# Optimization experiments

Measured on AMD Instinct MI355X. Metric: run time of the kernel, lower is better.

The kernel has to match this reference:

```python
import jax, jax.numpy as jnp
import numpy as np

NEG_INF = -1e30  # stands in for float('-inf'); avoids nan in masked softmax edge cases


def setup_inputs() -> dict:
    key = jax.random.key(0)
    ks = jax.random.split(key, 6)
    B, N, MD, QD, AD = 64, 512, 1024, 1024, 1024
    stdv_m = 1.0 / np.sqrt(MD)
    stdv_q = 1.0 / np.sqrt(QD)
    stdv_a = 1.0 / np.sqrt(AD)
    return {
        "memory_values": jax.random.normal(ks[0], (B, N, MD), dtype=jnp.float32),
        "mask": jax.random.randint(ks[1], (B, N), 0, 2, dtype=jnp.int32),
        "query": jax.random.normal(ks[2], (B, QD), dtype=jnp.float32),
        "Wh": jax.random.uniform(ks[3], (MD, AD), jnp.float32, -stdv_m, stdv_m),
        "Ws": jax.random.uniform(ks[4], (QD, AD), jnp.float32, -stdv_q, stdv_q),
        "v": jax.random.uniform(ks[5], (AD, 1), jnp.float32, -stdv_a, stdv_a),
    }


def reference(memory_values, mask, query, Wh, Ws, v):
    # Et(i) = tanh(Hi*Wh + St*Ws) @ v ; At = softmax(Et) with masking
    tq = query @ Ws                                   # (B, AD)
    h = jnp.tanh(memory_values @ Wh + tq[:, None, :])  # (B, N, AD)
    logits = jnp.squeeze(h @ v, axis=-1)              # (B, N)

    maskf = mask.astype(logits.dtype)
    # no_cells[b] == 1 iff every cell in row b is masked out
    no_cells = jnp.prod(1.0 - maskf, axis=1, keepdims=True)  # (B, 1)
    suppress = jnp.where(maskf == 0, NEG_INF, 0.0)
    suppress = jnp.where(no_cells == 1.0, 0.0, suppress)
    weights = jax.nn.softmax(logits + suppress, axis=-1)
    weights = jnp.where(no_cells == 1.0, 0.0, weights)

    context = jnp.einsum("bn,bnd->bd", weights, memory_values)
    return context
```

## Files before the change

### kernel.cpp

```cpp
#include <hip/hip_runtime.h>
#include <cstdint>
#include <cstddef>

typedef float floatx4 __attribute__((ext_vector_type(4)));
typedef _Float16 half8_t __attribute__((ext_vector_type(8)));
typedef _Float16 half2_t __attribute__((ext_vector_type(2)));

#define AS1 __attribute__((address_space(1)))
#define AS3 __attribute__((address_space(3)))

__device__ __forceinline__ void glds16(const void* g, void* l) {
  __builtin_amdgcn_global_load_lds((const AS1 void*)g, (AS3 void*)l, 16, 0, 0);
}

__device__ __forceinline__ half2_t pkrtz(float a, float b) {
  return __builtin_bit_cast(half2_t, __builtin_amdgcn_cvt_pkrtz(a, b));
}

__device__ __forceinline__ float fast_tanh(float x) {
  float e2 = __expf(2.f * x);
  return 1.f - 2.f * __builtin_amdgcn_rcpf(e2 + 1.f);
}

__global__ __launch_bounds__(256) void k_prep(
    const float* __restrict__ Wh, _Float16* __restrict__ WhT,
    const float* __restrict__ q, const float* __restrict__ Ws,
    float* __restrict__ tq) {
  __shared__ float sh[64 * 65];
  const int bx = blockIdx.x;
  const int tid = threadIdx.x;
  if (bx < 256) {
    int n0 = (bx & 15) << 6, k0 = (bx >> 4) << 6;
    int tx = tid & 63, ty = tid >> 6;
    #pragma unroll
    for (int r = ty; r < 64; r += 4) sh[r * 65 + tx] = Wh[(size_t)(k0 + r) * 1024 + n0 + tx];
    __syncthreads();
    #pragma unroll
    for (int r = ty; r < 64; r += 4)
      WhT[(size_t)(n0 + r) * 1024 + k0 + tx] = (_Float16)sh[tx * 65 + r];
  } else {
    int bb = bx - 256;
    int d0 = (bb & 15) << 6, b = bb >> 4;
    int dl = tid & 63, kg = tid >> 6;
    float* qs = sh;
    float* red = sh + 1024;
    for (int k = tid; k < 1024; k += 256) qs[k] = q[(b << 10) + k];
    __syncthreads();
    float acc = 0.f;
    int kbase = kg << 8;
    #pragma unroll 8
    for (int k = 0; k < 256; ++k)
      acc += qs[kbase + k] * Ws[(size_t)(kbase + k) * 1024 + d0 + dl];
    red[(kg << 6) + dl] = acc;
    __syncthreads();
    if (kg == 0)
      tq[(b << 10) + d0 + dl] = red[dl] + red[64 + dl] + red[128 + dl] + red[192 + dl];
  }
}

__global__ __launch_bounds__(512, 2) void k2_8ph(
    const float* __restrict__ Af, const _Float16* __restrict__ BT,
    const float* __restrict__ tq, const float* __restrict__ v,
    float* __restrict__ partials) {
  extern __shared__ char smem[];
  const int bid = blockIdx.x;
  const int wg = ((bid & 7) << 6) | (bid >> 3);
  const int mtile = wg >> 2, ntile = wg & 3;
  const int m0 = mtile << 8, n0 = ntile << 8;
  const int tid = threadIdx.x;
  const int w = tid >> 6, lane = tid & 63;
  const int wm = w >> 2, wn = w & 3, quad = lane >> 4, l15 = lane & 15;

  int aoff[2][4], boff[2][2];
  #pragma unroll
  for (int ks = 0; ks < 2; ++ks) {
    int swz = ((ks << 2) + quad) ^ (l15 & 7);
    #pragma unroll
    for (int i = 0; i < 4; ++i)
      aoff[ks][i] = (wm << 14) + (((i << 4) + l15) << 7) + (swz << 4);
    #pragma unroll
    for (int j = 0; j < 2; ++j)
      boff[ks][j] = 65536 + (wn << 12) + (((j << 4) + l15) << 7) + (swz << 4);
  }

  const int rr = tid >> 3, cc = tid & 7;
  const int r5 = rr & 31;
  int aSrcF[4];
  #pragma unroll
  for (int s = 0; s < 4; ++s)
    aSrcF[s] = ((m0 + ((s >> 1) << 7) + ((s & 1) << 6) + rr) << 10) + ((cc ^ (rr & 7)) << 3);
  const int awDst = tid << 4;

  int bSrc[2][2], dB[2][2];
  #pragma unroll
  for (int ch = 0; ch < 2; ++ch)
    #pragma unroll
    for (int is = 0; is < 2; ++is) {
      int wnb = (is << 1) + (rr >> 5);
      bSrc[ch][is] = ((n0 + (wnb << 6) + (ch << 5) + r5) << 10) + ((cc ^ (r5 & 7)) << 3);
      dB[ch][is] = 65536 + (ch << 14) + (is << 13) + (w << 10);
    }

  floatx4 acc[8][4];
  #pragma unroll
  for (int i = 0; i < 8; ++i)
    #pragma unroll
    for (int j = 0; j < 4; ++j) acc[i][j] = floatx4{0.f, 0.f, 0.f, 0.f};

  half8_t af[2][4], bf[2][2][2];
  floatx4 areg[4][2];

#define ALOADS(KST)                                                \
  _Pragma("unroll")                                                \
  for (int s_ = 0; s_ < 4; ++s_) {                                 \
    areg[s_][0] = *(const floatx4*)(Af + aSrcF[s_] + (KST));       \
    areg[s_][1] = *(const floatx4*)(Af + aSrcF[s_] + (KST) + 4);   \
  }                                                                \
  asm volatile("" ::: "memory");
#define AWRITE(OO)                                                 \
  _Pragma("unroll")                                                \
  for (int s_ = 0; s_ < 4; ++s_) {                                 \
    union { half2_t h2[4]; half8_t h8; } u_;                       \
    u_.h2[0] = pkrtz(areg[s_][0][0], areg[s_][0][1]);              \
    u_.h2[1] = pkrtz(areg[s_][0][2], areg[s_][0][3]);              \
    u_.h2[2] = pkrtz(areg[s_][1][0], areg[s_][1][1]);              \
    u_.h2[3] = pkrtz(areg[s_][1][2], areg[s_][1][3]);              \
    *(half8_t*)(smem + (OO) + (s_ << 13) + awDst) = u_.h8;         \
  }
#define STAGE_B(CH, KST, OO)                                  \
  glds16(BT + bSrc[CH][0] + (KST), smem + (OO) + dB[CH][0]);  \
  glds16(BT + bSrc[CH][1] + (KST), smem + (OO) + dB[CH][1]);
#define VM0 asm volatile("s_waitcnt vmcnt(0)" ::: "memory");
#define LGKM0 asm volatile("s_waitcnt lgkmcnt(0)" ::: "memory");
#define BAR __builtin_amdgcn_s_barrier();
#define LOAD_AF(CO, RHOFF)                                    \
  _Pragma("unroll")                                           \
  for (int ks_ = 0; ks_ < 2; ++ks_) {                         \
    _Pragma("unroll")                                         \
    for (int i_ = 0; i_ < 4; ++i_)                            \
      af[ks_][i_] = *(const half8_t*)(smem + (CO) + (RHOFF) + aoff[ks_][i_]); \
  }
#define LOAD_BF(CH, CO, CHOFF)                                \
  _Pragma("unroll")                                           \
  for (int ks_ = 0; ks_ < 2; ++ks_) {                         \
    _Pragma("unroll")                                         \
    for (int j_ = 0; j_ < 2; ++j_)                            \
      bf[CH][ks_][j_] = *(const half8_t*)(smem + (CO) + (CHOFF) + boff[ks_][j_]); \
  }
#define MFMAS(RH, CH)                                         \
  _Pragma("unroll")                                           \
  for (int ks_ = 0; ks_ < 2; ++ks_) {                         \
    _Pragma("unroll")                                         \
    for (int i_ = 0; i_ < 4; ++i_) {                          \
      _Pragma("unroll")                                       \
      for (int j_ = 0; j_ < 2; ++j_)                          \
        acc[(RH)*4 + i_][(CH)*2 + j_] = __builtin_amdgcn_mfma_f32_16x16x32_f16( \
            af[ks_][i_], bf[CH][ks_][j_], acc[(RH)*4 + i_][(CH)*2 + j_], 0, 0, 0); \
    }                                                         \
  }
#define PRIO_MFMA(RH, CH)                                     \
  __builtin_amdgcn_s_setprio(1);                              \
  MFMAS(RH, CH)                                               \
  __builtin_amdgcn_s_setprio(0);
#define GROUPT(CO, OO, KST)                                   \
                                                      \
  LOAD_AF(CO, 0)                                              \
  LOAD_BF(0, CO, 0)                                           \
  ALOADS(KST)                                                 \
  STAGE_B(0, KST, OO)                                         \
  STAGE_B(1, KST, OO)                                         \
  BAR                                                         \
  PRIO_MFMA(0, 0)                                             \
  BAR                                                         \
                                                      \
  LOAD_BF(1, CO, 16384)                                       \
  BAR                                                         \
  PRIO_MFMA(0, 1)                                             \
  BAR                                                         \
                                                      \
  AWRITE(OO)                                                  \
  LOAD_AF(CO, 8192)                                           \
  BAR                                                         \
  PRIO_MFMA(1, 0)                                             \
  BAR                                                         \
                                                      \
  LGKM0                                                       \
  VM0                                                         \
  BAR                                                         \
  PRIO_MFMA(1, 1)                                             \
  BAR

  ALOADS(0)
  STAGE_B(0, 0, 0)
  STAGE_B(1, 0, 0)
  AWRITE(0)
  LGKM0
  VM0
  BAR

  #pragma unroll 1
  for (int g2 = 0; g2 < 8; ++g2) {
    const int g = g2 << 1;
    const int kst1 = (g + 1) << 6;
    const int kst2 = (g2 == 7) ? (15 << 6) : ((g + 2) << 6);
    GROUPT(0, 32768, kst1)
    GROUPT(32768, 0, kst2)
  }

#undef GROUPT
#undef PRIO_MFMA
#undef MFMAS
#undef LOAD_BF
#undef LOAD_AF
#undef BAR
#undef LGKM0
#undef VM0
#undef STAGE_B
#undef AWRITE
#undef ALOADS

  asm volatile("s_waitcnt vmcnt(0)" ::: "memory");

  const int b = m0 >> 9;
  const int colb = n0 + (wn << 6) + l15;
  float tqv[4], vv[4];
  #pragma unroll
  for (int jf = 0; jf < 4; ++jf) {
    int n = colb + (jf << 4);
    tqv[jf] = tq[(b << 10) + n];
    vv[jf] = v[n];
  }
  #pragma unroll
  for (int rf = 0; rf < 8; ++rf) {
    #pragma unroll
    for (int r = 0; r < 4; ++r) {
      float s = 0.f;
      #pragma unroll
      for (int jf = 0; jf < 4; ++jf) s += fast_tanh(acc[rf][jf][r] + tqv[jf]) * vv[jf];
      s += __shfl_xor(s, 1);
      s += __shfl_xor(s, 2);
      s += __shfl_xor(s, 4);
      s += __shfl_xor(s, 8);
      if (l15 == 0) {
        int m = m0 + (wm << 7) + (rf << 4) + (quad << 2) + r;
        partials[m * 16 + (ntile << 2) + wn] = s;
      }
    }
  }
}

__global__ __launch_bounds__(256, 2) void k2_gemm_f32(
    const float* __restrict__ A, const _Float16* __restrict__ BT,
    const float* __restrict__ tq, const float* __restrict__ v,
    float* __restrict__ partials) {
  __shared__ float As[128 * 32];
  __shared__ _Float16 Bs[128 * 32];
  const int bid = blockIdx.x;
  const int mtile = ((bid >> 6) << 3) | (bid & 7);
  const int nblk = (bid >> 3) & 7;
  const int m0 = mtile << 7, n0 = nblk << 7;
  const int tid = threadIdx.x;
  const int w = tid >> 6, lane = tid & 63;
  const int wm = w >> 1, wn = w & 1, quad = lane >> 4, l15 = lane & 15;

  floatx4 acc[4][4];
  #pragma unroll
  for (int i = 0; i < 4; ++i)
    #pragma unroll
    for (int j = 0; j < 4; ++j) acc[i][j] = floatx4{0.f, 0.f, 0.f, 0.f};

  const float* gA[4];
  float* lA[4];
  #pragma unroll
  for (int t = 0; t < 4; ++t) {
    int L = (t << 8) + (w << 6) + lane;
    int row = L >> 3, jj = L & 7;
    int j = (jj - row) & 7;
    gA[t] = A + (size_t)(m0 + row) * 1024 + (j << 2);
    lA[t] = As + (t << 10) + (w << 8);
  }
  const _Float16* gB[2];
  _Float16* lB[2];
  #pragma unroll
  for (int t = 0; t < 2; ++t) {
    int L = (t << 8) + (w << 6) + lane;
    int row = L >> 2, jj = L & 3;
    int j = (jj - row - (row >> 2)) & 3;
    gB[t] = BT + (size_t)(n0 + row) * 1024 + (j << 3);
    lB[t] = Bs + (t << 11) + (w << 9);
  }
  const floatx4* aaddr[4][2];
  #pragma unroll
  for (int i = 0; i < 4; ++i) {
    int row = (wm << 6) + (i << 4) + l15;
    #pragma unroll
    for (int h = 0; h < 2; ++h) {
      int pos = ((quad << 1) + h + row) & 7;
      aaddr[i][h] = (const floatx4*)(As + (row << 5) + (pos << 2));
    }
  }
  const half8_t* baddr[4];
  #pragma unroll
  for (int j = 0; j < 4; ++j) {
    int row = (wn << 6) + (j << 4) + l15;
    int pos = (quad + row + (row >> 2)) & 3;
    baddr[j] = (const half8_t*)(Bs + (row << 5) + (pos << 3));
  }
  for (int k0 = 0; k0 < 1024; k0 += 32) {
    __syncthreads();
    glds16(gA[0] + k0, lA[0]);
    glds16(gA[1] + k0, lA[1]);
    glds16(gA[2] + k0, lA[2]);
    glds16(gA[3] + k0, lA[3]);
    glds16(gB[0] + k0, lB[0]);
    glds16(gB[1] + k0, lB[1]);
    __syncthreads();
    half8_t af[4], bfr[4];
    #pragma unroll
    for (int i = 0; i < 4; ++i) {
      floatx4 x = *aaddr[i][0], y = *aaddr[i][1];
      union { half2_t h2[4]; half8_t h8; } u;
      u.h2[0] = pkrtz(x[0], x[1]);
      u.h2[1] = pkrtz(x[2], x[3]);
      u.h2[2] = pkrtz(y[0], y[1]);
      u.h2[3] = pkrtz(y[2], y[3]);
      af[i] = u.h8;
    }
    #pragma unroll
    for (int j = 0; j < 4; ++j) bfr[j] = *baddr[j];
    #pragma unroll
    for (int i = 0; i < 4; ++i)
      #pragma unroll
      for (int j = 0; j < 4; ++j)
        acc[i][j] = __builtin_amdgcn_mfma_f32_16x16x32_f16(af[i], bfr[j], acc[i][j], 0, 0, 0);
  }
  const int b = m0 >> 9;
  const int colbase = n0 + (wn << 6) + l15;
  float tqv[4], vv[4];
  #pragma unroll
  for (int j = 0; j < 4; ++j) {
    int n = colbase + (j << 4);
    tqv[j] = tq[(b << 10) + n];
    vv[j] = v[n];
  }
  #pragma unroll
  for (int i = 0; i < 4; ++i) {
    #pragma unroll
    for (int r = 0; r < 4; ++r) {
      float s = 0.f;
      #pragma unroll
      for (int j = 0; j < 4; ++j) s += fast_tanh(acc[i][j][r] + tqv[j]) * vv[j];
      s += __shfl_xor(s, 1);
      s += __shfl_xor(s, 2);
      s += __shfl_xor(s, 4);
      s += __shfl_xor(s, 8);
      if (l15 == 0) {
        int m = m0 + (wm << 6) + (i << 4) + (quad << 2) + r;
        partials[m * 16 + (nblk << 1) + wn] = s;
      }
    }
  }
}

__global__ __launch_bounds__(512) void k3_softmax(const float* __restrict__ partials,
                                                  const int* __restrict__ mask,
                                                  float* __restrict__ weights) {
  int b = blockIdx.x;
  int n = threadIdx.x;
  int m = (b << 9) + n;
  float s = 0.f;
  #pragma unroll
  for (int i = 0; i < 16; ++i) s += partials[m * 16 + i];
  int mk = mask[m];
  float logit = mk ? s : -1e30f;
  __shared__ float red[8];
  float x = logit;
  #pragma unroll
  for (int off = 32; off > 0; off >>= 1) x = fmaxf(x, __shfl_xor(x, off));
  if ((n & 63) == 0) red[n >> 6] = x;
  __syncthreads();
  float mx = red[0];
  #pragma unroll
  for (int i = 1; i < 8; ++i) mx = fmaxf(mx, red[i]);
  float e = mk ? __expf(logit - mx) : 0.f;
  float ss = e;
  #pragma unroll
  for (int off = 32; off > 0; off >>= 1) ss += __shfl_xor(ss, off);
  __syncthreads();
  if ((n & 63) == 0) red[n >> 6] = ss;
  __syncthreads();
  float tot = 0.f;
  #pragma unroll
  for (int i = 0; i < 8; ++i) tot += red[i];
  weights[m] = (tot > 0.f) ? e / tot : 0.f;
}

__global__ void k4_ctx_f32(const float* __restrict__ mem, const float* __restrict__ weights,
                           float* __restrict__ ctxp) {
  int nc = blockIdx.x, b = blockIdx.y;
  int d = threadIdx.x << 3;
  floatx4 a0 = {0.f, 0.f, 0.f, 0.f}, a1 = {0.f, 0.f, 0.f, 0.f};
  int nbase = nc << 6;
  for (int n = nbase; n < nbase + 64; ++n) {
    float wv = weights[(b << 9) + n];
    const floatx4* p = (const floatx4*)(mem + ((size_t)((b << 9) + n) << 10) + d);
    a0 += wv * p[0];
    a1 += wv * p[1];
  }
  floatx4* o = (floatx4*)(ctxp + ((size_t)((b << 3) + nc) << 10) + d);
  o[0] = a0;
  o[1] = a1;
}

__global__ void k5_reduce8(const float* __restrict__ ctxp, float* __restrict__ out) {
  int i = (blockIdx.x << 8) + threadIdx.x;
  int b = i >> 10, d = i & 1023;
  float s = 0.f;
  #pragma unroll
  for (int cc = 0; cc < 8; ++cc) s += ctxp[((size_t)((b << 3) + cc) << 10) + d];
  out[i] = s;
}

extern "C" void kernel_launch(void* const* d_in, const int* in_sizes, int n_in,
                              void* d_out, int out_size, void* d_ws, size_t ws_size,
                              hipStream_t stream) {
  const float* mem = (const float*)d_in[0];
  const int* mask = (const int*)d_in[1];
  const float* query = (const float*)d_in[2];
  const float* Wh = (const float*)d_in[3];
  const float* Ws = (const float*)d_in[4];
  const float* v = (const float*)d_in[5];
  float* out = (float*)d_out;

  char* ws = (char*)d_ws;
  _Float16* WhT = (_Float16*)ws;
  float* partials = (float*)(ws + (2ull << 20));
  float* tq = (float*)(ws + (4ull << 20));
  float* weights = (float*)(ws + (4ull << 20) + (256 << 10));
  float* ctxp = (float*)(ws + ((size_t)9 << 19));

  static int use8 = -1;
  if (use8 < 0) {
    use8 = (hipFuncSetAttribute((const void*)k2_8ph,
                                hipFuncAttributeMaxDynamicSharedMemorySize,
                                131072) == hipSuccess) ? 1 : 0;
  }

  k_prep<<<1280, 256, 0, stream>>>(Wh, WhT, query, Ws, tq);
  if (use8)
    k2_8ph<<<512, 512, 131072, stream>>>(mem, WhT, tq, v, partials);
  else
    k2_gemm_f32<<<2048, 256, 0, stream>>>(mem, WhT, tq, v, partials);
  k3_softmax<<<64, 512, 0, stream>>>(partials, mask, weights);
  k4_ctx_f32<<<dim3(8, 64), 128, 0, stream>>>(mem, weights, ctxp);
  k5_reduce8<<<256, 256, 0, stream>>>(ctxp, out);
}
```

Baseline: 350.5 us.

## Double-buffer A global loads one stage ahead and transpose partials layout

Splits the A prefetch registers into two alternating buffers so each GEMM group issues A loads for the stage after next while converting the previous stage's A into LDS. The full vmcnt(0) wait is relaxed to vmcnt(8), so the A loads can stay in flight across a barrier and hide global load latency. The partial-logit buffer also changes from [m][16] to [16][m], which makes the writes and the softmax reads contiguous across lanes. In exchange it uses more VGPRs, which could hurt occupancy, and the vmcnt accounting must exactly match the issue order.

Measured after the change: 503.0 us. 1.43x slower.

```diff
diff --git a/kernel.cpp b/kernel.cpp
--- a/kernel.cpp
+++ b/kernel.cpp
@@ -108,29 +108,29 @@
     for (int j = 0; j < 4; ++j) acc[i][j] = floatx4{0.f, 0.f, 0.f, 0.f};
 
   half8_t af[2][4], bf[2][2][2];
-  floatx4 areg[4][2];
-
-#define ALOADS(KST)                                                \
+  floatx4 aregA[4][2], aregB[4][2];
+
+#define ALOADS(R, KST)                                             \
   _Pragma("unroll")                                                \
   for (int s_ = 0; s_ < 4; ++s_) {                                 \
-    areg[s_][0] = *(const floatx4*)(Af + aSrcF[s_] + (KST));       \
-    areg[s_][1] = *(const floatx4*)(Af + aSrcF[s_] + (KST) + 4);   \
+    R[s_][0] = *(const floatx4*)(Af + aSrcF[s_] + (KST));          \
+    R[s_][1] = *(const floatx4*)(Af + aSrcF[s_] + (KST) + 4);      \
   }                                                                \
   asm volatile("" ::: "memory");
-#define AWRITE(OO)                                                 \
+#define AWRITE(R, OO)                                              \
   _Pragma("unroll")                                                \
   for (int s_ = 0; s_ < 4; ++s_) {                                 \
     union { half2_t h2[4]; half8_t h8; } u_;                       \
-    u_.h2[0] = pkrtz(areg[s_][0][0], areg[s_][0][1]);              \
-    u_.h2[1] = pkrtz(areg[s_][0][2], areg[s_][0][3]);              \
-    u_.h2[2] = pkrtz(areg[s_][1][0], areg[s_][1][1]);              \
-    u_.h2[3] = pkrtz(areg[s_][1][2], areg[s_][1][3]);              \
+    u_.h2[0] = pkrtz(R[s_][0][0], R[s_][0][1]);                    \
+    u_.h2[1] = pkrtz(R[s_][0][2], R[s_][0][3]);                    \
+    u_.h2[2] = pkrtz(R[s_][1][0], R[s_][1][1]);                    \
+    u_.h2[3] = pkrtz(R[s_][1][2], R[s_][1][3]);                    \
     *(half8_t*)(smem + (OO) + (s_ << 13) + awDst) = u_.h8;         \
   }
 #define STAGE_B(CH, KST, OO)                                  \
   glds16(BT + bSrc[CH][0] + (KST), smem + (OO) + dB[CH][0]);  \
   glds16(BT + bSrc[CH][1] + (KST), smem + (OO) + dB[CH][1]);
-#define VM0 asm volatile("s_waitcnt vmcnt(0)" ::: "memory");
+#define VM8 asm volatile("s_waitcnt vmcnt(8)" ::: "memory");
 #define LGKM0 asm volatile("s_waitcnt lgkmcnt(0)" ::: "memory");
 #define BAR __builtin_amdgcn_s_barrier();
 #define LOAD_AF(CO, RHOFF)                                    \
@@ -162,13 +162,13 @@
   __builtin_amdgcn_s_setprio(1);                              \
   MFMAS(RH, CH)                                               \
   __builtin_amdgcn_s_setprio(0);
-#define GROUPT(CO, OO, KST)                                   \
+#define GROUPT(CO, OO, CONS, ISS, KSTB, KSTA)                 \
                                                       \
   LOAD_AF(CO, 0)                                              \
   LOAD_BF(0, CO, 0)                                           \
-  ALOADS(KST)                                                 \
-  STAGE_B(0, KST, OO)                                         \
-  STAGE_B(1, KST, OO)                                         \
+  STAGE_B(0, KSTB, OO)                                        \
+  STAGE_B(1, KSTB, OO)                                        \
+  ALOADS(ISS, KSTA)                                           \
   BAR                                                         \
   PRIO_MFMA(0, 0)                                             \
   BAR                                                         \
@@ -178,33 +178,36 @@
   PRIO_MFMA(0, 1)                                             \
   BAR                                                         \
                                                       \
-  AWRITE(OO)                                                  \
+  AWRITE(CONS, OO)                                            \
   LOAD_AF(CO, 8192)                                           \
   BAR                                                         \
   PRIO_MFMA(1, 0)                                             \
   BAR                                                         \
                                                       \
   LGKM0                                                       \
-  VM0                                                         \
+  VM8                                                         \
   BAR                                                         \
   PRIO_MFMA(1, 1)                                             \
   BAR
 
-  ALOADS(0)
+  ALOADS(aregA, 0)
   STAGE_B(0, 0, 0)
   STAGE_B(1, 0, 0)
-  AWRITE(0)
+  AWRITE(aregA, 0)
+  ALOADS(aregA, 64)
   LGKM0
-  VM0
+  VM8
   BAR
 
   #pragma unroll 1
   for (int g2 = 0; g2 < 8; ++g2) {
     const int g = g2 << 1;
-    const int kst1 = (g + 1) << 6;
-    const int kst2 = (g2 == 7) ? (15 << 6) : ((g + 2) << 6);
-    GROUPT(0, 32768, kst1)
-    GROUPT(32768, 0, kst2)
+    const int kb1 = (g + 1) << 6;
+    const int ka1 = ((g + 2) > 15 ? 15 : (g + 2)) << 6;
+    const int kb2 = ((g + 2) > 15 ? 15 : (g + 2)) << 6;
+    const int ka2 = ((g + 3) > 15 ? 15 : (g + 3)) << 6;
+    GROUPT(0, 32768, aregA, aregB, kb1, ka1)
+    GROUPT(32768, 0, aregB, aregA, kb2, ka2)
   }
 
 #undef GROUPT
@@ -214,7 +217,7 @@
 #undef LOAD_AF
 #undef BAR
 #undef LGKM0
-#undef VM0
+#undef VM8
 #undef STAGE_B
 #undef AWRITE
 #undef ALOADS
@@ -230,6 +233,7 @@
     tqv[jf] = tq[(b << 10) + n];
     vv[jf] = v[n];
   }
+  const int pcol = (ntile << 2) + wn;
   #pragma unroll
   for (int rf = 0; rf < 8; ++rf) {
     #pragma unroll
@@ -243,7 +247,7 @@
       s += __shfl_xor(s, 8);
       if (l15 == 0) {
         int m = m0 + (wm << 7) + (rf << 4) + (quad << 2) + r;
-        partials[m * 16 + (ntile << 2) + wn] = s;
+        partials[(pcol << 15) + m] = s;
       }
     }
   }
@@ -356,7 +360,7 @@
       s += __shfl_xor(s, 8);
       if (l15 == 0) {
         int m = m0 + (wm << 6) + (i << 4) + (quad << 2) + r;
-        partials[m * 16 + (nblk << 1) + wn] = s;
+        partials[(((nblk << 1) + wn) << 15) + m] = s;
       }
     }
   }
@@ -370,7 +374,7 @@
   int m = (b << 9) + n;
   float s = 0.f;
   #pragma unroll
-  for (int i = 0; i < 16; ++i) s += partials[m * 16 + i];
+  for (int i = 0; i < 16; ++i) s += partials[(i << 15) + m];
   int mk = mask[m];
   float logit = mk ? s : -1e30f;
   __shared__ float red[8];
```
